# Kernel optimization log

Hardware: AMD Instinct MI355X
Metric: run time of the kernel (lower is better)

The kernel has to match this reference:

```python
import jax, jax.numpy as jnp
import numpy as np


def _dct_last(x):
    # torch_dct along last axis: mirror-extend, forward-normalized FFT, sign(Re)*|X|
    L = x.shape[-1]
    arr = jnp.concatenate([x, x[..., ::-1]], axis=-1)
    X = jnp.fft.fft(arr, axis=-1, norm='forward')[..., :L]
    return jnp.abs(X) * jnp.sign(X.real)


def _dct_2d(x):
    row = _dct_last(x)
    col = _dct_last(jnp.swapaxes(row, -1, -2))
    return jnp.swapaxes(col, -1, -2)


def _dct_chan(x):
    # same transform along channel dim (axis 1)
    C = x.shape[1]
    arr = jnp.concatenate([x, x[:, ::-1]], axis=1)
    X = jnp.fft.fft(arr, axis=1, norm='forward')[:, :C]
    return jnp.abs(X) * jnp.sign(X.real)


def _idct_chan(x):
    # iDCT_Channel: shifted double-length spectrum -> ifft -> flipped real part
    B, C, H, W = x.shape
    v = jnp.arange(2 * C)
    shift = jnp.exp((-1j * 2.0 * jnp.pi * (C - 0.5) / (2 * C)) * v).astype(jnp.complex64)
    vi = x * (2.0 * C)
    flipneg = -vi[:, 1:][:, ::-1]                     # -flip(x[:,1:])
    full = jnp.concatenate([vi, jnp.zeros((B, 1, H, W), x.dtype), flipneg], axis=1)
    full = full.astype(jnp.complex64) * shift[None, :, None, None]
    xx = jnp.fft.ifft(full, axis=1)
    return xx[:, :C][:, ::-1].real


TOPK = 8
TOPK_CHANS = 8


def setup_inputs() -> dict:
    key = jax.random.key(0)
    k1, k2, k3, k4 = jax.random.split(key, 4)
    B, C, H, W = 4, 64, 256, 256
    red = 8
    return {
        'ip': jax.random.normal(k1, (B, C, H, W), dtype=jnp.float32),
        'fc1_w': jax.random.normal(k2, (C // red, C * TOPK), dtype=jnp.float32) * (1.0 / np.sqrt(C * TOPK)),
        'fc2_w': jax.random.normal(k3, (C, C // red), dtype=jnp.float32) * (1.0 / np.sqrt(C // red)),
        'conv_w': jax.random.normal(k4, (1, TOPK_CHANS, 3, 3), dtype=jnp.float32) * (1.0 / np.sqrt(TOPK_CHANS * 9)),
        'conv_b': jnp.zeros((1,), dtype=jnp.float32),
    }


def reference(ip, fc1_w, fc2_w, conv_w, conv_b):
    ip = ip.astype(jnp.float32)
    # channel-frequency attention
    ca = _dct_chan(ip)                                        # [B,C,H,W]
    ct = jnp.transpose(ca, (0, 2, 3, 1))                      # [B,H,W,C]
    topv = jax.lax.top_k(ct, TOPK_CHANS)[0]                   # [B,H,W,k]
    channel_topk = jnp.transpose(topv, (0, 3, 1, 2))          # [B,k,H,W]
    conv = jax.lax.conv_general_dilated(
        channel_topk, conv_w, (1, 1), 'SAME',
        dimension_numbers=('NCHW', 'OIHW', 'NCHW')) + conv_b[None, :, None, None]
    gate = jax.nn.sigmoid(conv)                               # [B,1,H,W]
    final = ca * gate
    x = _idct_chan(final).astype(jnp.float32)                 # [B,C,H,W]
    # spatial-DCT top-k channel gating MLP
    B, C = x.shape[0], x.shape[1]
    dct2 = _dct_2d(x).reshape(B, C, -1)                       # [B,C,H*W]
    topc = jax.lax.top_k(dct2, TOPK)[0].reshape(B, -1)        # [B,C*topk]
    h = jax.nn.relu(topc @ fc1_w.T)                           # [B,C//red]
    w = jax.nn.sigmoid(h @ fc2_w.T).reshape(B, C, 1, 1)       # [B,C,1,1]
    return x * w
```

## Files before the change

kernel.cpp:

```cpp
#include <hip/hip_runtime.h>
#include <hip/hip_bf16.h>
#include <math.h>

#define HW 65536
#define NCH 64
#define NB 4

typedef __attribute__((ext_vector_type(8))) short bf16x8;
typedef __attribute__((ext_vector_type(4))) float f32x4;
typedef __attribute__((ext_vector_type(8))) unsigned short u16x8;

__device__ inline unsigned short f2b(float f) {
  __hip_bfloat16 h = __float2bfloat16(f);
  return *(unsigned short*)&h;
}

__global__ void gen_tables(float* __restrict__ Mc,
                           unsigned short* __restrict__ Tb) {
  int i = blockIdx.x * 256 + threadIdx.x;
  const double PI = 3.14159265358979323846;
  if (i < 4096) {
    int k = i >> 6, c = i & 63;
    Mc[i] = (float)(cos(PI * (double)(k * (2 * c + 1)) / 128.0) / 64.0);
  }
  {
    int n = i >> 8, k = i & 255;
    float v = (float)(cos(PI * (double)(n * (2 * k + 1)) / 512.0) / 256.0);
    Tb[i] = f2b(v);
  }
}

__global__ __launch_bounds__(256) void gemm64(
    const float* __restrict__ Ag, int lda, long long sAb,
    const float* __restrict__ Bg, int ldb, long long sBb,
    float* __restrict__ Cg, int ldc, long long sCb, int K,
    const float* __restrict__ gate, long long sGb) {
  __shared__ float As[16][68];
  __shared__ float Bs[16][68];
  const int tid = threadIdx.x;
  const int tx = tid & 15, ty = tid >> 4;
  const int bn = blockIdx.x, bm = blockIdx.y, bz = blockIdx.z;
  const float* Ab = Ag + bz * sAb + (long long)bm * 64 * lda;
  const float* Bp = Bg + bz * sBb;
  const long long n0 = (long long)bn * 64;
  const int bcol = tid & 63;
  const int brow = tid >> 6;
  const int acol = tid & 15;
  const int arow = tid >> 4;
  float g = 1.0f;
  if (gate) g = gate[bz * sGb + n0 + bcol];
  float acc[4][4] = {{0.f}};

  for (int k0 = 0; k0 < K; k0 += 16) {
#pragma unroll
    for (int i = 0; i < 4; i++) {
      int r = arow + 16 * i;
      As[acol][r] = Ab[(long long)r * lda + (k0 + acol)];
    }
#pragma unroll
    for (int i = 0; i < 4; i++) {
      int r = brow + 4 * i;
      Bs[r][bcol] = Bp[(long long)(k0 + r) * ldb + n0 + bcol] * g;
    }
    __syncthreads();
#pragma unroll
    for (int kk = 0; kk < 16; kk++) {
      float4 a4 = *(const float4*)&As[kk][ty * 4];
      float4 b4 = *(const float4*)&Bs[kk][tx * 4];
      float a[4] = {a4.x, a4.y, a4.z, a4.w};
      float b[4] = {b4.x, b4.y, b4.z, b4.w};
#pragma unroll
      for (int i = 0; i < 4; i++)
#pragma unroll
        for (int j = 0; j < 4; j++) acc[i][j] = fmaf(a[i], b[j], acc[i][j]);
    }
    __syncthreads();
  }
#pragma unroll
  for (int i = 0; i < 4; i++) {
    float4 o;
    o.x = acc[i][0]; o.y = acc[i][1]; o.z = acc[i][2]; o.w = acc[i][3];
    *(float4*)&Cg[bz * sCb + (long long)(bm * 64 + ty * 4 + i) * ldc + n0 +
                  tx * 4] = o;
  }
}

__global__ __launch_bounds__(256) void top8_chan(const float* __restrict__ ca,
                                                 float* __restrict__ ct) {
  int gidx = blockIdx.x * 256 + threadIdx.x;
  int b = gidx >> 16, p = gidx & 65535;
  const float* src = ca + (long long)b * NCH * HW + p;
  float t[8];
#pragma unroll
  for (int j = 0; j < 8; j++) t[j] = -INFINITY;
  for (int c = 0; c < NCH; c++) {
    float v = src[(long long)c * HW];
#pragma unroll
    for (int q = 0; q < 8; q++) {
      if (v > t[q]) { float tmp = t[q]; t[q] = v; v = tmp; }
    }
  }
  float* dst = ct + (long long)b * 8 * HW + p;
#pragma unroll
  for (int j = 0; j < 8; j++) dst[(long long)j * HW] = t[j];
}

__global__ __launch_bounds__(256) void conv_gate(const float* __restrict__ ct,
                                                 const float* __restrict__ cw,
                                                 const float* __restrict__ cbias,
                                                 float* __restrict__ gate) {
  int gidx = blockIdx.x * 256 + threadIdx.x;
  int b = gidx >> 16, p = gidx & 65535;
  int h = p >> 8, w = p & 255;
  float acc = cbias[0];
#pragma unroll
  for (int j = 0; j < 8; j++) {
    const float* base = ct + ((long long)b * 8 + j) * HW;
#pragma unroll
    for (int dy = 0; dy < 3; dy++) {
      int y = h + dy - 1;
      if ((unsigned)y < 256u) {
#pragma unroll
        for (int dx = 0; dx < 3; dx++) {
          int x = w + dx - 1;
          if ((unsigned)x < 256u)
            acc += base[y * 256 + x] * cw[j * 9 + dy * 3 + dx];
        }
      }
    }
  }
  gate[gidx] = 1.0f / (1.0f + expf(-acc));
}

__global__ __launch_bounds__(256) void mfma_rowdct(
    const float* __restrict__ ip, const float* __restrict__ gateb,
    const unsigned short* __restrict__ Tb, unsigned short* __restrict__ Rt) {
  __shared__ unsigned short As[128][40];
  __shared__ unsigned short Bs[128][40];
  const int tid = threadIdx.x;
  const int m0 = blockIdx.y * 128;
  const int n0 = blockIdx.x * 128;
  const int wv = tid >> 6, lane = tid & 63;
  const int wr = wv >> 1, wc = wv & 1;
  const int l15 = lane & 15, kb = lane >> 4;
  const int srow = tid & 127, sseg = tid >> 7;
  f32x4 acc[4][4] = {};

  for (int k0 = 0; k0 < 256; k0 += 32) {
    {
      const int r = m0 + srow;
      const int h = r & 255;
      const int b = r >> 14;
      const float* p  = ip + (long long)r * 256 + k0 + sseg * 8;
      const float* gp = gateb + ((long long)b << 16) + (h << 8) + k0 + sseg * 8;
      float4 v0 = *(const float4*)p,  v1 = *(const float4*)(p + 4);
      float4 g0 = *(const float4*)gp, g1 = *(const float4*)(gp + 4);
      u16x8 w;
      w[0] = f2b(v0.x * g0.x); w[1] = f2b(v0.y * g0.y);
      w[2] = f2b(v0.z * g0.z); w[3] = f2b(v0.w * g0.w);
      w[4] = f2b(v1.x * g1.x); w[5] = f2b(v1.y * g1.y);
      w[6] = f2b(v1.z * g1.z); w[7] = f2b(v1.w * g1.w);
      *(u16x8*)&As[srow][sseg * 8] = w;
    }
    *(u16x8*)&Bs[srow][sseg * 8] =
        *(const u16x8*)(Tb + (n0 + srow) * 256 + k0 + sseg * 8);
    __syncthreads();
    bf16x8 a[4], b[4];
#pragma unroll
    for (int mi = 0; mi < 4; mi++)
      a[mi] = *(const bf16x8*)&As[wr * 64 + mi * 16 + l15][kb * 8];
#pragma unroll
    for (int ni = 0; ni < 4; ni++)
      b[ni] = *(const bf16x8*)&Bs[wc * 64 + ni * 16 + l15][kb * 8];
#pragma unroll
    for (int mi = 0; mi < 4; mi++)
#pragma unroll
      for (int ni = 0; ni < 4; ni++)
        acc[mi][ni] = __builtin_amdgcn_mfma_f32_16x16x32_bf16(
            a[mi], b[ni], acc[mi][ni], 0, 0, 0);
    __syncthreads();
  }

  const int img = m0 >> 8;
  const int hb = (m0 & 255) + wr * 64 + kb * 4;
#pragma unroll
  for (int mi = 0; mi < 4; mi++) {
#pragma unroll
    for (int ni = 0; ni < 4; ni++) {
      int h = hb + mi * 16;
      int n = n0 + wc * 64 + ni * 16 + l15;
      ushort4 o;
      o.x = f2b(acc[mi][ni][0]); o.y = f2b(acc[mi][ni][1]);
      o.z = f2b(acc[mi][ni][2]); o.w = f2b(acc[mi][ni][3]);
      *(ushort4*)&Rt[(long long)img * 65536 + (long long)n * 256 + h] = o;
    }
  }
}

__global__ __launch_bounds__(256) void mfma_coldct_top8(
    const unsigned short* __restrict__ Tb, const unsigned short* __restrict__ Rt,
    float* __restrict__ top8out) {
  __shared__ unsigned short As[128][40];
  __shared__ unsigned short Bs[128][40];
  __shared__ float lists[256 * 8];
  const int tid = threadIdx.x;
  const int m0 = blockIdx.y * 128;
  const int n0 = blockIdx.x * 128;
  const int img = blockIdx.z;
  const int wv = tid >> 6, lane = tid & 63;
  const int wr = wv >> 1, wc = wv & 1;
  const int l15 = lane & 15, kb = lane >> 4;
  const int srow = tid & 127, sseg = tid >> 7;
  const unsigned short* Rb = Rt + (long long)img * 65536;
  f32x4 acc[4][4] = {};

  for (int k0 = 0; k0 < 256; k0 += 32) {
    *(u16x8*)&As[srow][sseg * 8] =
        *(const u16x8*)(Tb + (m0 + srow) * 256 + k0 + sseg * 8);
    *(u16x8*)&Bs[srow][sseg * 8] =
        *(const u16x8*)(Rb + (n0 + srow) * 256 + k0 + sseg * 8);
    __syncthreads();
    bf16x8 a[4], b[4];
#pragma unroll
    for (int mi = 0; mi < 4; mi++)
      a[mi] = *(const bf16x8*)&As[wr * 64 + mi * 16 + l15][kb * 8];
#pragma unroll
    for (int ni = 0; ni < 4; ni++)
      b[ni] = *(const bf16x8*)&Bs[wc * 64 + ni * 16 + l15][kb * 8];
#pragma unroll
    for (int mi = 0; mi < 4; mi++)
#pragma unroll
      for (int ni = 0; ni < 4; ni++)
        acc[mi][ni] = __builtin_amdgcn_mfma_f32_16x16x32_bf16(
            a[mi], b[ni], acc[mi][ni], 0, 0, 0);
    __syncthreads();
  }

  float t[8];
#pragma unroll
  for (int j = 0; j < 8; j++) t[j] = -INFINITY;
#pragma unroll
  for (int mi = 0; mi < 4; mi++)
#pragma unroll
    for (int ni = 0; ni < 4; ni++)
#pragma unroll
      for (int j = 0; j < 4; j++) {
        float v = acc[mi][ni][j];
#pragma unroll
        for (int q = 0; q < 8; q++) {
          if (v > t[q]) { float tmp = t[q]; t[q] = v; v = tmp; }
        }
      }
#pragma unroll
  for (int j = 0; j < 8; j++) lists[tid * 8 + j] = t[j];
  __syncthreads();
  for (int s = 128; s >= 1; s >>= 1) {
    if (tid < s) {
      int ii = 0, jj = 0;
      float out[8];
#pragma unroll
      for (int m = 0; m < 8; m++) {
        float av = lists[tid * 8 + ii];
        float bv = lists[(tid + s) * 8 + jj];
        bool ta = (av >= bv);
        out[m] = ta ? av : bv;
        ii += ta ? 1 : 0;
        jj += ta ? 0 : 1;
      }
#pragma unroll
      for (int m = 0; m < 8; m++) lists[tid * 8 + m] = out[m];
    }
    __syncthreads();
  }
  if (tid < 8) {
    long long idx = ((long long)img * gridDim.y + blockIdx.y) * gridDim.x +
                    blockIdx.x;
    top8out[idx * 8 + tid] = lists[tid];
  }
}

__global__ void merge_top8(const float* __restrict__ lists,
                           float* __restrict__ topc) {
  int img = blockIdx.x * 64 + threadIdx.x;
  if (img >= 256) return;
  float t[8];
#pragma unroll
  for (int j = 0; j < 8; j++) t[j] = -INFINITY;
  for (int l = 0; l < 4; l++) {
#pragma unroll
    for (int m = 0; m < 8; m++) {
      float v = lists[(img * 4 + l) * 8 + m];
#pragma unroll
      for (int q = 0; q < 8; q++) {
        if (v > t[q]) { float tmp = t[q]; t[q] = v; v = tmp; }
      }
    }
  }
  int b = img >> 6, c = img & 63;
#pragma unroll
  for (int j = 0; j < 8; j++) topc[b * 512 + c * 8 + j] = t[j];
}

__global__ void mlp_kernel(const float* __restrict__ topc,
                           const float* __restrict__ fc1,
                           const float* __restrict__ fc2,
                           float* __restrict__ wout) {
  __shared__ float hbuf[32];
  int tid = threadIdx.x;
  if (tid < 32) {
    int b = tid >> 3, i = tid & 7;
    float acc = 0.f;
    for (int j = 0; j < 512; j++) acc += topc[b * 512 + j] * fc1[i * 512 + j];
    hbuf[tid] = fmaxf(acc, 0.f);
  }
  __syncthreads();
  int b = tid >> 6, c = tid & 63;
  float acc = 0.f;
#pragma unroll
  for (int i = 0; i < 8; i++) acc += hbuf[b * 8 + i] * fc2[c * 8 + i];
  wout[tid] = 1.0f / (1.0f + expf(-acc));
}

__global__ __launch_bounds__(256) void final_scale(
    const float* __restrict__ ip, const float* __restrict__ gateb,
    const float* __restrict__ wfin, float* __restrict__ out) {
  long long i = ((long long)blockIdx.x * 256 + threadIdx.x) * 4;
  int bc = (int)(i >> 16);
  int b = bc >> 6;
  int p = (int)(i & 65535);
  float4 v = *(const float4*)&ip[i];
  float4 g = *(const float4*)&gateb[((long long)b << 16) + p];
  float s = wfin[bc];
  v.x *= g.x * s; v.y *= g.y * s; v.z *= g.z * s; v.w *= g.w * s;
  *(float4*)&out[i] = v;
}

extern "C" void kernel_launch(void* const* d_in, const int* in_sizes, int n_in,
                              void* d_out, int out_size, void* d_ws,
                              size_t ws_size, hipStream_t stream) {
  (void)in_sizes; (void)n_in; (void)out_size; (void)ws_size;
  const float* ip  = (const float*)d_in[0];
  const float* fc1 = (const float*)d_in[1];
  const float* fc2 = (const float*)d_in[2];
  const float* cw  = (const float*)d_in[3];
  const float* cb  = (const float*)d_in[4];
  float* out = (float*)d_out;
  float* ws = (float*)d_ws;

  float* Mc     = ws;
  unsigned short* Tb = (unsigned short*)(ws + 8192);
  float* gateb  = ws + 139264;
  float* wfin   = ws + 401408;
  float* topc   = ws + 401664;
  float* listsb = ws + 403712;
  float* ca     = ws + 1048576;
  float* ct8    = ws + 1048576 + 16777216;

  const long long CHW = (long long)NCH * HW;

  gen_tables<<<256, 256, 0, stream>>>(Mc, Tb);

  gemm64<<<dim3(1024, 1, 4), 256, 0, stream>>>(
      Mc, 64, 0, ip, HW, CHW, ca, HW, CHW, 64, nullptr, 0);

  top8_chan<<<1024, 256, 0, stream>>>(ca, ct8);
  conv_gate<<<1024, 256, 0, stream>>>(ct8, cw, cb, gateb);

  unsigned short* Rt = (unsigned short*)ca;
  mfma_rowdct<<<dim3(2, 512), 256, 0, stream>>>(ip, gateb, Tb, Rt);

  mfma_coldct_top8<<<dim3(2, 2, 256), 256, 0, stream>>>(Tb, Rt, listsb);

  merge_top8<<<4, 64, 0, stream>>>(listsb, topc);
  mlp_kernel<<<1, 256, 0, stream>>>(topc, fc1, fc2, wfin);

  final_scale<<<16384, 256, 0, stream>>>(ip, gateb, wfin, out);
}
```

Before: 296.5 us.

## Fuse channel DCT with top-8 selection, prefetch GEMM tiles, use shuffle-based top-8 merge

The channel-DCT GEMM now computes per-pixel top-8 over channels in its epilogue through shared memory. This removes the 64MB intermediate ca write and the separate top8_chan kernel that re-read it. Both MFMA DCT kernels gain register prefetch of the next K-slice, so global loads overlap the MFMA work. The block-level top-8 reduction is replaced by a branchless merge8 network over wave shuffles, removing many syncthreads. These changes add shared memory and register pressure.

```diff
diff --git a/kernel.cpp b/kernel.cpp
--- a/kernel.cpp
+++ b/kernel.cpp
@@ -13,6 +13,19 @@
 __device__ inline unsigned short f2b(float f) {
   __hip_bfloat16 h = __float2bfloat16(f);
   return *(unsigned short*)&h;
+}
+
+__device__ inline void merge8(float A[8], const float B[8]) {
+  float M[8];
+#pragma unroll
+  for (int i = 0; i < 8; i++) {
+    float m = fmaxf(A[i], B[i]);
+#pragma unroll
+    for (int j = 0; j < i; j++) m = fmaxf(m, fminf(A[j], B[i - 1 - j]));
+    M[i] = m;
+  }
+#pragma unroll
+  for (int i = 0; i < 8; i++) A[i] = M[i];
 }
 
 __global__ void gen_tables(float* __restrict__ Mc,
@@ -30,37 +43,34 @@
   }
 }
 
-__global__ __launch_bounds__(256) void gemm64(
-    const float* __restrict__ Ag, int lda, long long sAb,
-    const float* __restrict__ Bg, int ldb, long long sBb,
-    float* __restrict__ Cg, int ldc, long long sCb, int K,
-    const float* __restrict__ gate, long long sGb) {
+__global__ __launch_bounds__(256) void chan_gemm_top8(
+    const float* __restrict__ ip, const float* __restrict__ Mc,
+    float* __restrict__ ct) {
   __shared__ float As[16][68];
   __shared__ float Bs[16][68];
+  __shared__ float T[64][69];
+  __shared__ float lists[64][33];
   const int tid = threadIdx.x;
   const int tx = tid & 15, ty = tid >> 4;
-  const int bn = blockIdx.x, bm = blockIdx.y, bz = blockIdx.z;
-  const float* Ab = Ag + bz * sAb + (long long)bm * 64 * lda;
-  const float* Bp = Bg + bz * sBb;
+  const int bn = blockIdx.x, bz = blockIdx.z;
+  const float* Bp = ip + (long long)bz * NCH * HW;
   const long long n0 = (long long)bn * 64;
   const int bcol = tid & 63;
   const int brow = tid >> 6;
   const int acol = tid & 15;
   const int arow = tid >> 4;
-  float g = 1.0f;
-  if (gate) g = gate[bz * sGb + n0 + bcol];
   float acc[4][4] = {{0.f}};
 
-  for (int k0 = 0; k0 < K; k0 += 16) {
+  for (int k0 = 0; k0 < 64; k0 += 16) {
 #pragma unroll
     for (int i = 0; i < 4; i++) {
       int r = arow + 16 * i;
-      As[acol][r] = Ab[(long long)r * lda + (k0 + acol)];
+      As[acol][r] = Mc[r * 64 + (k0 + acol)];
     }
 #pragma unroll
     for (int i = 0; i < 4; i++) {
       int r = brow + 4 * i;
-      Bs[r][bcol] = Bp[(long long)(k0 + r) * ldb + n0 + bcol] * g;
+      Bs[r][bcol] = Bp[(long long)(k0 + r) * HW + n0 + bcol];
     }
     __syncthreads();
 #pragma unroll
@@ -76,33 +86,46 @@
     }
     __syncthreads();
   }
-#pragma unroll
-  for (int i = 0; i < 4; i++) {
-    float4 o;
-    o.x = acc[i][0]; o.y = acc[i][1]; o.z = acc[i][2]; o.w = acc[i][3];
-    *(float4*)&Cg[bz * sCb + (long long)(bm * 64 + ty * 4 + i) * ldc + n0 +
-                  tx * 4] = o;
-  }
-}
-
-__global__ __launch_bounds__(256) void top8_chan(const float* __restrict__ ca,
-                                                 float* __restrict__ ct) {
-  int gidx = blockIdx.x * 256 + threadIdx.x;
-  int b = gidx >> 16, p = gidx & 65535;
-  const float* src = ca + (long long)b * NCH * HW + p;
-  float t[8];
-#pragma unroll
-  for (int j = 0; j < 8; j++) t[j] = -INFINITY;
-  for (int c = 0; c < NCH; c++) {
-    float v = src[(long long)c * HW];
-#pragma unroll
-    for (int q = 0; q < 8; q++) {
-      if (v > t[q]) { float tmp = t[q]; t[q] = v; v = tmp; }
-    }
-  }
-  float* dst = ct + (long long)b * 8 * HW + p;
-#pragma unroll
-  for (int j = 0; j < 8; j++) dst[(long long)j * HW] = t[j];
+
+#pragma unroll
+  for (int j = 0; j < 4; j++) {
+    int pix = tx * 4 + j;
+#pragma unroll
+    for (int i = 0; i < 4; i++) T[pix][ty * 4 + i] = acc[i][j];
+  }
+  __syncthreads();
+  {
+    int pix = tid & 63, q = tid >> 6;
+    float t8[8];
+#pragma unroll
+    for (int j = 0; j < 8; j++) t8[j] = -INFINITY;
+#pragma unroll
+    for (int c = 0; c < 16; c++) {
+      float v = T[pix][q * 16 + c];
+#pragma unroll
+      for (int s = 0; s < 8; s++) {
+        if (v > t8[s]) { float tmp = t8[s]; t8[s] = v; v = tmp; }
+      }
+    }
+#pragma unroll
+    for (int j = 0; j < 8; j++) lists[pix][q * 8 + j] = t8[j];
+  }
+  __syncthreads();
+  if (tid < 64) {
+    float A8[8];
+#pragma unroll
+    for (int j = 0; j < 8; j++) A8[j] = lists[tid][j];
+#pragma unroll
+    for (int q = 1; q < 4; q++) {
+      float B8[8];
+#pragma unroll
+      for (int j = 0; j < 8; j++) B8[j] = lists[tid][q * 8 + j];
+      merge8(A8, B8);
+    }
+    float* dst = ct + (long long)bz * 8 * HW + n0 + tid;
+#pragma unroll
+    for (int j = 0; j < 8; j++) dst[(long long)j * HW] = A8[j];
+  }
 }
 
 __global__ __launch_bounds__(256) void conv_gate(const float* __restrict__ ct,
@@ -144,27 +167,33 @@
   const int wr = wv >> 1, wc = wv & 1;
   const int l15 = lane & 15, kb = lane >> 4;
   const int srow = tid & 127, sseg = tid >> 7;
+  const int r = m0 + srow;
+  const int hh = r & 255;
+  const int bb = r >> 14;
+  const float* p  = ip + (long long)r * 256 + sseg * 8;
+  const float* gp = gateb + ((long long)bb << 16) + (hh << 8) + sseg * 8;
+  const unsigned short* tp = Tb + (n0 + srow) * 256 + sseg * 8;
   f32x4 acc[4][4] = {};
 
-  for (int k0 = 0; k0 < 256; k0 += 32) {
-    {
-      const int r = m0 + srow;
-      const int h = r & 255;
-      const int b = r >> 14;
-      const float* p  = ip + (long long)r * 256 + k0 + sseg * 8;
-      const float* gp = gateb + ((long long)b << 16) + (h << 8) + k0 + sseg * 8;
-      float4 v0 = *(const float4*)p,  v1 = *(const float4*)(p + 4);
-      float4 g0 = *(const float4*)gp, g1 = *(const float4*)(gp + 4);
-      u16x8 w;
-      w[0] = f2b(v0.x * g0.x); w[1] = f2b(v0.y * g0.y);
-      w[2] = f2b(v0.z * g0.z); w[3] = f2b(v0.w * g0.w);
-      w[4] = f2b(v1.x * g1.x); w[5] = f2b(v1.y * g1.y);
-      w[6] = f2b(v1.z * g1.z); w[7] = f2b(v1.w * g1.w);
-      *(u16x8*)&As[srow][sseg * 8] = w;
-    }
-    *(u16x8*)&Bs[srow][sseg * 8] =
-        *(const u16x8*)(Tb + (n0 + srow) * 256 + k0 + sseg * 8);
-    __syncthreads();
+  float4 v0 = *(const float4*)p,  v1 = *(const float4*)(p + 4);
+  float4 g0 = *(const float4*)gp, g1 = *(const float4*)(gp + 4);
+  u16x8 rT = *(const u16x8*)tp;
+
+  for (int it = 0; it < 8; ++it) {
+    u16x8 w;
+    w[0] = f2b(v0.x * g0.x); w[1] = f2b(v0.y * g0.y);
+    w[2] = f2b(v0.z * g0.z); w[3] = f2b(v0.w * g0.w);
+    w[4] = f2b(v1.x * g1.x); w[5] = f2b(v1.y * g1.y);
+    w[6] = f2b(v1.z * g1.z); w[7] = f2b(v1.w * g1.w);
+    *(u16x8*)&As[srow][sseg * 8] = w;
+    *(u16x8*)&Bs[srow][sseg * 8] = rT;
+    __syncthreads();
+    if (it < 7) {
+      int o = (it + 1) * 32;
+      v0 = *(const float4*)(p + o);  v1 = *(const float4*)(p + o + 4);
+      g0 = *(const float4*)(gp + o); g1 = *(const float4*)(gp + o + 4);
+      rT = *(const u16x8*)(tp + o);
+    }
     bf16x8 a[4], b[4];
 #pragma unroll
     for (int mi = 0; mi < 4; mi++)
@@ -202,7 +231,7 @@
     float* __restrict__ top8out) {
   __shared__ unsigned short As[128][40];
   __shared__ unsigned short Bs[128][40];
-  __shared__ float lists[256 * 8];
+  __shared__ float wl[4][8];
   const int tid = threadIdx.x;
   const int m0 = blockIdx.y * 128;
   const int n0 = blockIdx.x * 128;
@@ -211,15 +240,22 @@
   const int wr = wv >> 1, wc = wv & 1;
   const int l15 = lane & 15, kb = lane >> 4;
   const int srow = tid & 127, sseg = tid >> 7;
-  const unsigned short* Rb = Rt + (long long)img * 65536;
+  const unsigned short* Ap = Tb + (m0 + srow) * 256 + sseg * 8;
+  const unsigned short* Bp = Rt + (long long)img * 65536 + (n0 + srow) * 256 +
+                             sseg * 8;
   f32x4 acc[4][4] = {};
 
-  for (int k0 = 0; k0 < 256; k0 += 32) {
-    *(u16x8*)&As[srow][sseg * 8] =
-        *(const u16x8*)(Tb + (m0 + srow) * 256 + k0 + sseg * 8);
-    *(u16x8*)&Bs[srow][sseg * 8] =
-        *(const u16x8*)(Rb + (n0 + srow) * 256 + k0 + sseg * 8);
-    __syncthreads();
+  u16x8 rA = *(const u16x8*)Ap;
+  u16x8 rB = *(const u16x8*)Bp;
+
+  for (int it = 0; it < 8; ++it) {
+    *(u16x8*)&As[srow][sseg * 8] = rA;
+    *(u16x8*)&Bs[srow][sseg * 8] = rB;
+    __syncthreads();
+    if (it < 7) {
+      rA = *(const u16x8*)(Ap + (it + 1) * 32);
+      rB = *(const u16x8*)(Bp + (it + 1) * 32);
+    }
     bf16x8 a[4], b[4];
 #pragma unroll
     for (int mi = 0; mi < 4; mi++)
@@ -236,9 +272,9 @@
     __syncthreads();
   }
 
-  float t[8];
-#pragma unroll
-  for (int j = 0; j < 8; j++) t[j] = -INFINITY;
+  float t8[8];
+#pragma unroll
+  for (int j = 0; j < 8; j++) t8[j] = -INFINITY;
 #pragma unroll
   for (int mi = 0; mi < 4; mi++)
 #pragma unroll
@@ -248,34 +284,33 @@
         float v = acc[mi][ni][j];
 #pragma unroll
         for (int q = 0; q < 8; q++) {
-          if (v > t[q]) { float tmp = t[q]; t[q] = v; v = tmp; }
+          if (v > t8[q]) { float tmp = t8[q]; t8[q] = v; v = tmp; }
         }
       }
 #pragma unroll
-  for (int j = 0; j < 8; j++) lists[tid * 8 + j] = t[j];
+  for (int st = 1; st < 64; st <<= 1) {
+    float B8[8];
+#pragma unroll
+    for (int j = 0; j < 8; j++) B8[j] = __shfl_xor(t8[j], st, 64);
+    merge8(t8, B8);
+  }
+  if (lane == 0) {
+#pragma unroll
+    for (int j = 0; j < 8; j++) wl[wv][j] = t8[j];
+  }
   __syncthreads();
-  for (int s = 128; s >= 1; s >>= 1) {
-    if (tid < s) {
-      int ii = 0, jj = 0;
-      float out[8];
-#pragma unroll
-      for (int m = 0; m < 8; m++) {
-        float av = lists[tid * 8 + ii];
-        float bv = lists[(tid + s) * 8 + jj];
-        bool ta = (av >= bv);
-        out[m] = ta ? av : bv;
-        ii += ta ? 1 : 0;
-        jj += ta ? 0 : 1;
-      }
-#pragma unroll
-      for (int m = 0; m < 8; m++) lists[tid * 8 + m] = out[m];
-    }
-    __syncthreads();
-  }
-  if (tid < 8) {
+  if (tid == 0) {
+#pragma unroll
+    for (int w = 1; w < 4; w++) {
+      float B8[8];
+#pragma unroll
+      for (int j = 0; j < 8; j++) B8[j] = wl[w][j];
+      merge8(t8, B8);
+    }
     long long idx = ((long long)img * gridDim.y + blockIdx.y) * gridDim.x +
                     blockIdx.x;
-    top8out[idx * 8 + tid] = lists[tid];
+#pragma unroll
+    for (int j = 0; j < 8; j++) top8out[idx * 8 + j] = t8[j];
   }
 }
 
@@ -353,20 +388,15 @@
   float* wfin   = ws + 401408;
   float* topc   = ws + 401664;
   float* listsb = ws + 403712;
-  float* ca     = ws + 1048576;
+  float* big    = ws + 1048576;
   float* ct8    = ws + 1048576 + 16777216;
 
-  const long long CHW = (long long)NCH * HW;
-
   gen_tables<<<256, 256, 0, stream>>>(Mc, Tb);
 
-  gemm64<<<dim3(1024, 1, 4), 256, 0, stream>>>(
-      Mc, 64, 0, ip, HW, CHW, ca, HW, CHW, 64, nullptr, 0);
-
-  top8_chan<<<1024, 256, 0, stream>>>(ca, ct8);
+  chan_gemm_top8<<<dim3(1024, 1, 4), 256, 0, stream>>>(ip, Mc, ct8);
   conv_gate<<<1024, 256, 0, stream>>>(ct8, cw, cb, gateb);
 
-  unsigned short* Rt = (unsigned short*)ca;
+  unsigned short* Rt = (unsigned short*)big;
   mfma_rowdct<<<dim3(2, 512), 256, 0, stream>>>(ip, gateb, Tb, Rt);
 
   mfma_coldct_top8<<<dim3(2, 2, 256), 256, 0, stream>>>(Tb, Rt, listsb);
```

Result: faster. 282.3 us (-4.8%).
